# Kernel optimization log

Hardware: AMD Instinct MI355X
Metric: run time of the kernel (lower is better)

Reference implementation:

```python
import jax, jax.numpy as jnp
import numpy as np

T, H, I, E, K = 1024, 1024, 1024, 16, 4
ALPHA, LIMIT, EPS = 1.702, 7.0, 1e-5


def setup_inputs() -> dict:
    key = jax.random.key(0)
    ks = jax.random.split(key, 8)
    return {
        "x": jax.random.normal(ks[0], (T, H), jnp.float32),
        "norm_w": jnp.ones((H,), jnp.float32) + 0.01 * jax.random.normal(ks[1], (H,), jnp.float32),
        "router_w": 0.02 * jax.random.normal(ks[2], (E, H), jnp.float32),
        "router_b": jnp.zeros((E,), jnp.float32),
        "w13": 0.02 * jax.random.normal(ks[3], (E, H, 2 * I), jnp.float32),
        "b13": 0.01 * jax.random.normal(ks[4], (E, 2 * I), jnp.float32),
        "w2": 0.02 * jax.random.normal(ks[5], (E, I, H), jnp.float32),
        "b2": 0.01 * jax.random.normal(ks[6], (E, H), jnp.float32),
        "manual_weights": jnp.zeros((1, E), jnp.float32),  # zeros => override branch inactive, as in __init__
        "layer_idx": 0,
    }


def _override(g, lw):
    # torch: log_softmax, then force pos-masked experts to max+0.01, neg-masked to min-0.01
    gl = jax.nn.log_softmax(g, axis=-1)
    mx = jnp.max(gl, axis=-1, keepdims=True)
    mn = jnp.min(gl, axis=-1, keepdims=True)
    gl = jnp.where((lw > 0)[None, :], mx + 0.01, gl)
    gl = jnp.where((lw < 0)[None, :], mn - 0.01, gl)
    return gl


def reference(x, norm_w, router_w, router_b, w13, b13, w2, b2, manual_weights, layer_idx):
    # RMSNorm (eps=1e-5)
    t = x * jax.lax.rsqrt(jnp.mean(x * x, axis=-1, keepdims=True) + EPS) * norm_w
    # router logits [T, E]
    g = t @ router_w.T + router_b
    # conditional manual logit override
    lw = manual_weights[layer_idx]
    g = jax.lax.cond(jnp.max(jnp.abs(lw)) > 0,
                     lambda gg: _override(gg, lw),
                     lambda gg: gg, g)
    # top-k routing, renormalize=True (softmax -> topk -> renorm)
    probs = jax.nn.softmax(g, axis=-1)
    topw, topi = jax.lax.top_k(probs, K)
    topw = topw / jnp.sum(topw, axis=-1, keepdims=True)
    # dense combine matrix [T, E] (sparse dispatch in the fused kernel)
    combine = jnp.zeros(g.shape, x.dtype).at[jnp.arange(g.shape[0])[:, None], topi].add(topw)
    # expert compute: gate_up GEMM + swigluoai + down GEMM (dense over experts for the reference)
    h = jnp.einsum('th,ehf->tef', t, w13) + b13          # [T, E, 2I]
    gate = jnp.minimum(h[..., :I], LIMIT)                # clamp(max=limit)
    up = jnp.clip(h[..., I:], -LIMIT, LIMIT)             # clamp(-limit, limit)
    act = (up + 1.0) * gate * jax.nn.sigmoid(ALPHA * gate)
    y = jnp.einsum('tei,eih->teh', act, w2) + b2         # [T, E, H]
    moe = jnp.einsum('te,teh->th', combine, y)           # weighted scatter-combine
    return x + moe
```

## Files before the change

kernel.cpp:

```cpp
#include <hip/hip_runtime.h>

#define T_    1024
#define H_    1024
#define IDIM  1024
#define E_    16
#define TOPK  4
#define ALPHA 1.702f
#define LIMIT 7.0f

typedef __bf16 bf16;
typedef __bf16 bf16x4 __attribute__((ext_vector_type(4)));
typedef __bf16 bf16x8 __attribute__((ext_vector_type(8)));
typedef float  f32x4  __attribute__((ext_vector_type(4)));

__global__ __launch_bounds__(256) void k_rms_router(
    const float* __restrict__ x, const float* __restrict__ nw,
    const float* __restrict__ rw, const float* __restrict__ rb,
    const float* __restrict__ mw, const int* __restrict__ lidx,
    bf16* __restrict__ tB, float* __restrict__ out,
    int* __restrict__ cnt, int* __restrict__ tok_list,
    float* __restrict__ wgt_list)
{
    const int t = blockIdx.x, tid = threadIdx.x;
    const int lane = tid & 63, wave = tid >> 6;
    __shared__ float tbuf[H_];
    __shared__ float red[4];
    __shared__ float logits[E_];

    float4 xv = ((const float4*)(x + (size_t)t * H_))[tid];
    float4 wv = ((const float4*)nw)[tid];
    float ssq = xv.x*xv.x + xv.y*xv.y + xv.z*xv.z + xv.w*xv.w;
    #pragma unroll
    for (int off = 32; off; off >>= 1) ssq += __shfl_xor(ssq, off);
    if (lane == 0) red[wave] = ssq;
    __syncthreads();
    const float rms = rsqrtf((red[0] + red[1] + red[2] + red[3]) * (1.0f / H_) + 1e-5f);

    float4 tv;
    tv.x = xv.x * rms * wv.x;
    tv.y = xv.y * rms * wv.y;
    tv.z = xv.z * rms * wv.z;
    tv.w = xv.w * rms * wv.w;

    ((float4*)(out + (size_t)t * H_))[tid] = xv;
    ((float4*)tbuf)[tid] = tv;
    bf16x4 tb = { (bf16)tv.x, (bf16)tv.y, (bf16)tv.z, (bf16)tv.w };
    *(bf16x4*)(tB + (size_t)t * H_ + tid * 4) = tb;
    __syncthreads();

    #pragma unroll
    for (int ei = 0; ei < 4; ++ei) {
        const int e = wave * 4 + ei;
        const float* wr = rw + (size_t)e * H_;
        float s = 0.f;
        #pragma unroll
        for (int j = 0; j < 16; ++j) {
            const int c = lane + j * 64;
            s += tbuf[c] * wr[c];
        }
        #pragma unroll
        for (int off = 32; off; off >>= 1) s += __shfl_xor(s, off);
        if (lane == 0) logits[e] = s + rb[e];
    }
    __syncthreads();

    if (tid == 0) {
        float g[E_];
        #pragma unroll
        for (int e = 0; e < E_; ++e) g[e] = logits[e];

        const int li = lidx[0];
        float ma = 0.f, lw[E_];
        #pragma unroll
        for (int e = 0; e < E_; ++e) { lw[e] = mw[li * E_ + e]; ma = fmaxf(ma, fabsf(lw[e])); }
        if (ma > 0.f) {
            float mx = -1e30f;
            for (int e = 0; e < E_; ++e) mx = fmaxf(mx, g[e]);
            float se = 0.f;
            for (int e = 0; e < E_; ++e) se += expf(g[e] - mx);
            const float lse = logf(se) + mx;
            float gl[E_], gmx = -1e30f, gmn = 1e30f;
            for (int e = 0; e < E_; ++e) { gl[e] = g[e] - lse; gmx = fmaxf(gmx, gl[e]); gmn = fminf(gmn, gl[e]); }
            for (int e = 0; e < E_; ++e) {
                if (lw[e] > 0.f)      gl[e] = gmx + 0.01f;
                else if (lw[e] < 0.f) gl[e] = gmn - 0.01f;
                g[e] = gl[e];
            }
        }

        float mx = -1e30f;
        #pragma unroll
        for (int e = 0; e < E_; ++e) mx = fmaxf(mx, g[e]);
        float p[E_];
        #pragma unroll
        for (int e = 0; e < E_; ++e) p[e] = expf(g[e] - mx);

        bool used[E_] = {};
        int   idx[TOPK];
        float twv[TOPK];
        float ssum = 0.f;
        for (int k = 0; k < TOPK; ++k) {
            int best = -1; float bv = -1e30f;
            for (int e = 0; e < E_; ++e)
                if (!used[e] && p[e] > bv) { bv = p[e]; best = e; }
            used[best] = true; idx[k] = best; twv[k] = bv; ssum += bv;
        }
        const float inv = 1.f / ssum;
        for (int k = 0; k < TOPK; ++k) {
            const int e = idx[k];
            const int slot = atomicAdd(&cnt[e], 1);
            tok_list[e * T_ + slot] = t;
            wgt_list[e * T_ + slot] = twv[k] * inv;
        }
    }
}

__global__ void k_scan(const int* __restrict__ cnt, int* __restrict__ base,
                       int* __restrict__ tiln, int* __restrict__ tile_e,
                       int* __restrict__ tile_m0)
{
    if (threadIdx.x == 0) {
        int s = 0, nt = 0;
        for (int e = 0; e < E_; ++e) {
            base[e] = s; s += cnt[e];
            for (int m0 = 0; m0 < cnt[e]; m0 += 64) {
                if (nt < 96) { tile_e[nt] = e; tile_m0[nt] = m0; ++nt; }
            }
        }
        base[E_] = s;
        tiln[0] = nt;
    }
}

__global__ __launch_bounds__(256) void k_repack(
    const float* __restrict__ W, bf16* __restrict__ out, int Ndim)
{
    __shared__ float tile[32][260];
    const int e = blockIdx.z, kb = blockIdx.y, n0 = blockIdx.x * 256;
    const int t = threadIdx.x;
    const int nbs = Ndim >> 4;

    const float* src = W + ((size_t)e * 1024 + (size_t)kb * 32) * Ndim + n0;
    #pragma unroll
    for (int i = 0; i < 8; ++i) {
        const int idx = i * 256 + t;
        const int k = idx >> 6, c4 = (idx & 63) * 4;
        float4 v = *(const float4*)(src + (size_t)k * Ndim + c4);
        *(float4*)&tile[k][c4] = v;
    }
    __syncthreads();

    const int f = t >> 4;
    const int lg = (t & 15) * 4;
    bf16* dst = out + (((size_t)(e * nbs + n0 / 16 + f)) * 32 + kb) * 512;
    #pragma unroll
    for (int li = 0; li < 4; ++li) {
        const int l = lg + li, q = l >> 4, r = l & 15;
        bf16x8 p;
        #pragma unroll
        for (int j = 0; j < 8; ++j) p[j] = (bf16)tile[q * 8 + j][f * 16 + r];
        *(bf16x8*)(dst + l * 8) = p;
    }
}

__global__ __launch_bounds__(256) void k_gateup3(
    const bf16* __restrict__ tB, const bf16* __restrict__ w13p,
    const float* __restrict__ b13, const int* __restrict__ cnt,
    const int* __restrict__ base, const int* __restrict__ tiln,
    const int* __restrict__ tile_e, const int* __restrict__ tile_m0,
    const int* __restrict__ tok_list, bf16* __restrict__ act)
{
    const int ti = blockIdx.y;
    if (ti >= tiln[0]) return;
    const int e  = tile_e[ti];
    const int m0 = tile_m0[ti];
    const int ne = cnt[e];

    const int tid = threadIdx.x, lane = tid & 63, wave = tid >> 6;
    const int q = lane >> 4, r = lane & 15;

    __shared__ __align__(16) bf16 As[8 * 64 * 8];

    const int m   = tid >> 2, kq = tid & 3;
    const int mf_s = m >> 4, r_s = m & 15;
    const int kc_s = kq >> 1, q_s = (kq & 1) * 2;
    bf16* wr0 = As + ((size_t)((mf_s * 2 + kc_s) * 64 + q_s * 16 + r_s)) * 8;
    bf16* wr1 = wr0 + 16 * 8;
    int srow = m0 + m; srow = srow < ne ? srow : ne - 1;
    const bf16* pA = tB + (size_t)tok_list[e * T_ + srow] * H_ + kq * 16;

    const int nb_g = blockIdx.x * 4 + wave;
    const bf16* pBg = w13p + ((size_t)(e * 128 + nb_g     ) * 32) * 512 + lane * 8;
    const bf16* pBu = w13p + ((size_t)(e * 128 + nb_g + 64) * 32) * 512 + lane * 8;

    f32x4 accg[4] = {};
    f32x4 accu[4] = {};
    uint4 ar0a, ar0b, ar1a, ar1b;
    bf16x8 bg0[2], bu0[2], bg1[2], bu1[2];

#define LOADA(A0, A1) do { \
    A0 = *(const uint4*)pA; A1 = *(const uint4*)(pA + 8); pA += 64; } while (0)
#define STAGEA(A0, A1) do { \
    *(uint4*)wr0 = A0; *(uint4*)wr1 = A1; } while (0)
#define LOADB(BG, BU) do { \
    BG[0] = *(const bf16x8*)pBg; BG[1] = *(const bf16x8*)(pBg + 512); pBg += 1024; \
    BU[0] = *(const bf16x8*)pBu; BU[1] = *(const bf16x8*)(pBu + 512); pBu += 1024; } while (0)
#define COMPUTE(BG, BU) do { \
    _Pragma("unroll") \
    for (int kc = 0; kc < 2; ++kc) { \
        bf16x8 afr[4]; \
        _Pragma("unroll") \
        for (int mf = 0; mf < 4; ++mf) \
            afr[mf] = *(const bf16x8*)(As + ((size_t)((mf * 2 + kc) * 64 + lane)) * 8); \
        _Pragma("unroll") \
        for (int mf = 0; mf < 4; ++mf) { \
            accg[mf] = __builtin_amdgcn_mfma_f32_16x16x32_bf16(afr[mf], BG[kc], accg[mf], 0, 0, 0); \
            accu[mf] = __builtin_amdgcn_mfma_f32_16x16x32_bf16(afr[mf], BU[kc], accu[mf], 0, 0, 0); \
        } \
    } } while (0)

    LOADA(ar0a, ar0b);
    LOADB(bg0, bu0);
    #pragma unroll 2
    for (int kb = 0; kb < 16; kb += 2) {
        __syncthreads();
        STAGEA(ar0a, ar0b);
        LOADA(ar1a, ar1b);
        LOADB(bg1, bu1);
        __syncthreads();
        COMPUTE(bg0, bu0);

        __syncthreads();
        STAGEA(ar1a, ar1b);
        LOADA(ar0a, ar0b);
        LOADB(bg0, bu0);
        __syncthreads();
        COMPUTE(bg1, bu1);
    }
#undef LOADA
#undef STAGEA
#undef LOADB
#undef COMPUTE

    const int sb = base[e];
    const int cg = nb_g * 16 + r;
    const float bgv = b13[e * 2 * IDIM + cg];
    const float buv = b13[e * 2 * IDIM + IDIM + cg];
    #pragma unroll
    for (int mf = 0; mf < 4; ++mf) {
        #pragma unroll
        for (int rg = 0; rg < 4; ++rg) {
            const int row = mf * 16 + q * 4 + rg;
            if (m0 + row < ne) {
                const float hg = accg[mf][rg] + bgv;
                const float hu = accu[mf][rg] + buv;
                const float gt = fminf(hg, LIMIT);
                const float up = fminf(fmaxf(hu, -LIMIT), LIMIT);
                const float av = (up + 1.0f) * gt / (1.0f + expf(-ALPHA * gt));
                act[(size_t)(sb + m0 + row) * IDIM + cg] = (bf16)av;
            }
        }
    }
}

__global__ __launch_bounds__(256) void k_down3(
    const bf16* __restrict__ act, const bf16* __restrict__ w2p,
    const float* __restrict__ b2, const int* __restrict__ cnt,
    const int* __restrict__ base, const int* __restrict__ tiln,
    const int* __restrict__ tile_e, const int* __restrict__ tile_m0,
    const int* __restrict__ tok_list, const float* __restrict__ wgt_list,
    float* __restrict__ out)
{
    const int ti = blockIdx.y;
    if (ti >= tiln[0]) return;
    const int e  = tile_e[ti];
    const int m0 = tile_m0[ti];
    const int ne = cnt[e];
    const int sb = base[e];

    const int tid = threadIdx.x, lane = tid & 63, wave = tid >> 6;
    const int q = lane >> 4, r = lane & 15;

    __shared__ __align__(16) bf16 As[8 * 64 * 8];

    const int m   = tid >> 2, kq = tid & 3;
    const int mf_s = m >> 4, r_s = m & 15;
    const int kc_s = kq >> 1, q_s = (kq & 1) * 2;
    bf16* wr0 = As + ((size_t)((mf_s * 2 + kc_s) * 64 + q_s * 16 + r_s)) * 8;
    bf16* wr1 = wr0 + 16 * 8;
    int srow = m0 + m; srow = srow < ne ? srow : ne - 1;
    const bf16* pA = act + (size_t)(sb + srow) * IDIM + kq * 16;

    const int nb0 = blockIdx.x * 8 + wave * 2;
    const bf16* pB0 = w2p + ((size_t)(e * 64 + nb0    ) * 32) * 512 + lane * 8;
    const bf16* pB1 = w2p + ((size_t)(e * 64 + nb0 + 1) * 32) * 512 + lane * 8;

    f32x4 acc[4][2] = {};
    uint4 ar0a, ar0b, ar1a, ar1b;
    bf16x8 bA0[2], bB0[2], bA1[2], bB1[2];

#define LOADA(A0, A1) do { \
    A0 = *(const uint4*)pA; A1 = *(const uint4*)(pA + 8); pA += 64; } while (0)
#define STAGEA(A0, A1) do { \
    *(uint4*)wr0 = A0; *(uint4*)wr1 = A1; } while (0)
#define LOADB(B0, B1) do { \
    B0[0] = *(const bf16x8*)pB0; B0[1] = *(const bf16x8*)(pB0 + 512); pB0 += 1024; \
    B1[0] = *(const bf16x8*)pB1; B1[1] = *(const bf16x8*)(pB1 + 512); pB1 += 1024; } while (0)
#define COMPUTE(B0, B1) do { \
    _Pragma("unroll") \
    for (int kc = 0; kc < 2; ++kc) { \
        bf16x8 afr[4]; \
        _Pragma("unroll") \
        for (int mf = 0; mf < 4; ++mf) \
            afr[mf] = *(const bf16x8*)(As + ((size_t)((mf * 2 + kc) * 64 + lane)) * 8); \
        _Pragma("unroll") \
        for (int mf = 0; mf < 4; ++mf) { \
            acc[mf][0] = __builtin_amdgcn_mfma_f32_16x16x32_bf16(afr[mf], B0[kc], acc[mf][0], 0, 0, 0); \
            acc[mf][1] = __builtin_amdgcn_mfma_f32_16x16x32_bf16(afr[mf], B1[kc], acc[mf][1], 0, 0, 0); \
        } \
    } } while (0)

    LOADA(ar0a, ar0b);
    LOADB(bA0, bB0);
    #pragma unroll 2
    for (int kb = 0; kb < 16; kb += 2) {
        __syncthreads();
        STAGEA(ar0a, ar0b);
        LOADA(ar1a, ar1b);
        LOADB(bA1, bB1);
        __syncthreads();
        COMPUTE(bA0, bB0);

        __syncthreads();
        STAGEA(ar1a, ar1b);
        LOADA(ar0a, ar0b);
        LOADB(bA0, bB0);
        __syncthreads();
        COMPUTE(bA1, bB1);
    }
#undef LOADA
#undef STAGEA
#undef LOADB
#undef COMPUTE

    #pragma unroll
    for (int nf = 0; nf < 2; ++nf) {
        const int ch = (nb0 + nf) * 16 + r;
        const float bb = b2[e * H_ + ch];
        #pragma unroll
        for (int mf = 0; mf < 4; ++mf) {
            #pragma unroll
            for (int rg = 0; rg < 4; ++rg) {
                const int row = mf * 16 + q * 4 + rg;
                const int s = m0 + row;
                if (s < ne) {
                    const int   tok = tok_list[e * T_ + s];
                    const float w   = wgt_list[e * T_ + s];
                    atomicAdd(&out[(size_t)tok * H_ + ch], w * (acc[mf][nf][rg] + bb));
                }
            }
        }
    }
}

__global__ __launch_bounds__(256) void k_gateup(
    const bf16* __restrict__ tB, const float* __restrict__ w13,
    const float* __restrict__ b13, const int* __restrict__ cnt,
    const int* __restrict__ base, const int* __restrict__ tok_list,
    bf16* __restrict__ act)
{
    const int e  = blockIdx.z;
    const int ne = cnt[e];
    const int m0 = blockIdx.y * 64;
    if (m0 >= ne) return;
    const int n0  = blockIdx.x * 64;
    const int tid = threadIdx.x, lane = tid & 63, wave = tid >> 6;

    __shared__ __align__(16) bf16 As[64][40];
    __shared__ __align__(16) bf16 Bg[64][40];
    __shared__ __align__(16) bf16 Bu[64][40];
    __shared__ int stok[64];

    if (tid < 64) {
        const int s = m0 + tid;
        stok[tid] = (s < ne) ? tok_list[e * T_ + s] : -1;
    }
    __syncthreads();

    const int ar = tid >> 2, ak = (tid & 3) * 8;
    const int atok = stok[ar];
    const int bn = tid & 63, bk = wave * 8;
    const size_t wrow = (size_t)(2 * IDIM);
    const float* wbase = w13 + (size_t)e * H_ * wrow + n0 + bn;

    const int wm = wave >> 1, wn = wave & 1;
    const int q = lane >> 4, r = lane & 15;
    f32x4 accg[2][2] = {};
    f32x4 accu[2][2] = {};

    for (int kb = 0; kb < H_ / 32; ++kb) {
        __syncthreads();
        uint4 av = make_uint4(0u, 0u, 0u, 0u);
        if (atok >= 0)
            av = *(const uint4*)(tB + (size_t)atok * H_ + kb * 32 + ak);
        *(uint4*)&As[ar][ak] = av;
        {
            const float* src = wbase + (size_t)(kb * 32 + bk) * wrow;
            bf16x8 pg, pu;
            #pragma unroll
            for (int j = 0; j < 8; ++j) {
                pg[j] = (bf16)src[(size_t)j * wrow];
                pu[j] = (bf16)src[(size_t)j * wrow + IDIM];
            }
            *(bf16x8*)&Bg[bn][bk] = pg;
            *(bf16x8*)&Bu[bn][bk] = pu;
        }
        __syncthreads();
        bf16x8 a[2], bg[2], bu[2];
        a[0]  = *(const bf16x8*)&As[wm * 32 +      r][q * 8];
        a[1]  = *(const bf16x8*)&As[wm * 32 + 16 + r][q * 8];
        bg[0] = *(const bf16x8*)&Bg[wn * 32 +      r][q * 8];
        bg[1] = *(const bf16x8*)&Bg[wn * 32 + 16 + r][q * 8];
        bu[0] = *(const bf16x8*)&Bu[wn * 32 +      r][q * 8];
        bu[1] = *(const bf16x8*)&Bu[wn * 32 + 16 + r][q * 8];
        #pragma unroll
        for (int im = 0; im < 2; ++im)
            #pragma unroll
            for (int in = 0; in < 2; ++in) {
                accg[im][in] = __builtin_amdgcn_mfma_f32_16x16x32_bf16(a[im], bg[in], accg[im][in], 0, 0, 0);
                accu[im][in] = __builtin_amdgcn_mfma_f32_16x16x32_bf16(a[im], bu[in], accu[im][in], 0, 0, 0);
            }
    }

    const int sb = base[e];
    #pragma unroll
    for (int im = 0; im < 2; ++im)
        #pragma unroll
        for (int in = 0; in < 2; ++in)
            #pragma unroll
            for (int rg = 0; rg < 4; ++rg) {
                const int row = wm * 32 + im * 16 + q * 4 + rg;
                const int col = wn * 32 + in * 16 + r;
                if (m0 + row < ne) {
                    const float hg = accg[im][in][rg] + b13[e * 2 * IDIM + n0 + col];
                    const float hu = accu[im][in][rg] + b13[e * 2 * IDIM + IDIM + n0 + col];
                    const float gt = fminf(hg, LIMIT);
                    const float up = fminf(fmaxf(hu, -LIMIT), LIMIT);
                    const float av = (up + 1.0f) * gt / (1.0f + expf(-ALPHA * gt));
                    act[(size_t)(sb + m0 + row) * IDIM + n0 + col] = (bf16)av;
                }
            }
}

__global__ __launch_bounds__(256) void k_down(
    const bf16* __restrict__ act, const float* __restrict__ w2,
    const float* __restrict__ b2, const int* __restrict__ cnt,
    const int* __restrict__ base, const int* __restrict__ tok_list,
    const float* __restrict__ wgt_list, float* __restrict__ out)
{
    const int e  = blockIdx.z;
    const int ne = cnt[e];
    const int m0 = blockIdx.y * 64;
    if (m0 >= ne) return;
    const int n0  = blockIdx.x * 64;
    const int tid = threadIdx.x, lane = tid & 63, wave = tid >> 6;

    __shared__ __align__(16) bf16 As[64][40];
    __shared__ __align__(16) bf16 Bs[64][40];
    __shared__ int   stok[64];
    __shared__ float swgt[64];

    if (tid < 64) {
        const int s = m0 + tid;
        stok[tid] = (s < ne) ? tok_list[e * T_ + s] : -1;
        swgt[tid] = (s < ne) ? wgt_list[e * T_ + s] : 0.f;
    }
    __syncthreads();

    const int sb = base[e];
    const int ar = tid >> 2, ak = (tid & 3) * 8;
    const bool arow_ok = (m0 + ar) < ne;
    const int bn = tid & 63, bk = wave * 8;
    const float* wbase = w2 + (size_t)e * IDIM * H_ + n0 + bn;

    const int wm = wave >> 1, wn = wave & 1;
    const int q = lane >> 4, r = lane & 15;
    f32x4 acc[2][2] = {};

    for (int kb = 0; kb < IDIM / 32; ++kb) {
        __syncthreads();
        uint4 av = make_uint4(0u, 0u, 0u, 0u);
        if (arow_ok)
            av = *(const uint4*)(act + (size_t)(sb + m0 + ar) * IDIM + kb * 32 + ak);
        *(uint4*)&As[ar][ak] = av;
        {
            const float* src = wbase + (size_t)(kb * 32 + bk) * H_;
            bf16x8 pb;
            #pragma unroll
            for (int j = 0; j < 8; ++j) pb[j] = (bf16)src[(size_t)j * H_];
            *(bf16x8*)&Bs[bn][bk] = pb;
        }
        __syncthreads();
        bf16x8 a[2], b[2];
        a[0] = *(const bf16x8*)&As[wm * 32 +      r][q * 8];
        a[1] = *(const bf16x8*)&As[wm * 32 + 16 + r][q * 8];
        b[0] = *(const bf16x8*)&Bs[wn * 32 +      r][q * 8];
        b[1] = *(const bf16x8*)&Bs[wn * 32 + 16 + r][q * 8];
        #pragma unroll
        for (int im = 0; im < 2; ++im)
            #pragma unroll
            for (int in = 0; in < 2; ++in)
                acc[im][in] = __builtin_amdgcn_mfma_f32_16x16x32_bf16(a[im], b[in], acc[im][in], 0, 0, 0);
    }

    #pragma unroll
    for (int im = 0; im < 2; ++im)
        #pragma unroll
        for (int in = 0; in < 2; ++in)
            #pragma unroll
            for (int rg = 0; rg < 4; ++rg) {
                const int row = wm * 32 + im * 16 + q * 4 + rg;
                const int col = wn * 32 + in * 16 + r;
                if (m0 + row < ne) {
                    const int   tok = stok[row];
                    const float w   = swgt[row];
                    atomicAdd(&out[(size_t)tok * H_ + n0 + col], w * (acc[im][in][rg] + b2[e * H_ + n0 + col]));
                }
            }
}

extern "C" void kernel_launch(void* const* d_in, const int* in_sizes, int n_in,
                              void* d_out, int out_size, void* d_ws, size_t ws_size,
                              hipStream_t stream)
{
    const float* x        = (const float*)d_in[0];
    const float* norm_w   = (const float*)d_in[1];
    const float* router_w = (const float*)d_in[2];
    const float* router_b = (const float*)d_in[3];
    const float* w13      = (const float*)d_in[4];
    const float* b13      = (const float*)d_in[5];
    const float* w2       = (const float*)d_in[6];
    const float* b2       = (const float*)d_in[7];
    const float* manual_w = (const float*)d_in[8];
    const int*   layer_i  = (const int*)d_in[9];
    float* out = (float*)d_out;

    char* ws = (char*)d_ws;
    bf16*  tB   = (bf16*)ws;
    bf16*  act  = (bf16*)(ws + (2ull << 20));
    char*  meta = ws + (10ull << 20);
    int*   cnt      = (int*)meta;
    int*   basep    = (int*)(meta + 64);
    int*   tiln     = (int*)(meta + 256);
    int*   tile_e   = (int*)(meta + 512);
    int*   tile_m0  = (int*)(meta + 1024);
    int*   tok_list = (int*)(meta + (16ull << 10));
    float* wgt_list = (float*)(meta + (16ull << 10) + (64ull << 10));
    bf16*  w13p     = (bf16*)(ws + (12ull << 20));
    bf16*  w2p      = (bf16*)(ws + (76ull << 20));

    const bool fast = ws_size >= (108ull << 20);

    hipMemsetAsync(cnt, 0, E_ * sizeof(int), stream);

    k_rms_router<<<T_, 256, 0, stream>>>(x, norm_w, router_w, router_b,
                                         manual_w, layer_i, tB, out,
                                         cnt, tok_list, wgt_list);
    k_scan<<<1, 64, 0, stream>>>(cnt, basep, tiln, tile_e, tile_m0);

    if (fast) {
        dim3 gr13(2 * IDIM / 256, 32, E_);
        k_repack<<<gr13, 256, 0, stream>>>(w13, w13p, 2 * IDIM);
        dim3 gr2(H_ / 256, 32, E_);
        k_repack<<<gr2, 256, 0, stream>>>(w2, w2p, H_);

        dim3 gg(16, 80);
        k_gateup3<<<gg, 256, 0, stream>>>(tB, w13p, b13, cnt, basep, tiln,
                                          tile_e, tile_m0, tok_list, act);
        dim3 gd(8, 80);
        k_down3<<<gd, 256, 0, stream>>>(act, w2p, b2, cnt, basep, tiln,
                                        tile_e, tile_m0, tok_list, wgt_list, out);
    } else {
        dim3 gg(IDIM / 64, T_ / 64, E_);
        k_gateup<<<gg, 256, 0, stream>>>(tB, w13, b13, cnt, basep, tok_list, act);
        dim3 gd(H_ / 64, T_ / 64, E_);
        k_down<<<gd, 256, 0, stream>>>(act, w2, b2, cnt, basep, tok_list, wgt_list, out);
    }
}
```

Baseline: 402.6 us.

## Drop weight repack kernels and load fp32 weights directly in MoE GEMMs

Removes the two per-call repack kernels that converted the fp32 expert weights into an MFMA-friendly bf16 layout. The GEMM kernels now read the fp32 weights in place with strided scalar loads, converting to bf16 in registers. This saves a full read and write of all weights each call, but replaces vectorized loads with many strided scalar ones. The K loop is peeled so it no longer issues the redundant final prefetch, and the single-thread scan becomes a wave shuffle prefix scan.

Result: slower. 452.3 us (+12.3%).

```diff
diff --git a/kernel.cpp b/kernel.cpp
--- a/kernel.cpp
+++ b/kernel.cpp
@@ -119,52 +119,36 @@
                        int* __restrict__ tiln, int* __restrict__ tile_e,
                        int* __restrict__ tile_m0)
 {
-    if (threadIdx.x == 0) {
-        int s = 0, nt = 0;
-        for (int e = 0; e < E_; ++e) {
-            base[e] = s; s += cnt[e];
-            for (int m0 = 0; m0 < cnt[e]; m0 += 64) {
-                if (nt < 96) { tile_e[nt] = e; tile_m0[nt] = m0; ++nt; }
-            }
-        }
-        base[E_] = s;
-        tiln[0] = nt;
+    const int lane = threadIdx.x;
+    int c = (lane < E_) ? cnt[lane] : 0;
+
+    int s = c;
+    #pragma unroll
+    for (int off = 1; off < 16; off <<= 1) {
+        int tv = __shfl_up(s, off);
+        if ((lane & 15) >= off) s += tv;
+    }
+    if (lane < E_) base[lane] = s - c;
+    if (lane == E_ - 1) base[E_] = s;
+
+    int nt = (lane < E_) ? ((c + 63) >> 6) : 0;
+    int ts = nt;
+    #pragma unroll
+    for (int off = 1; off < 16; off <<= 1) {
+        int tv = __shfl_up(ts, off);
+        if ((lane & 15) >= off) ts += tv;
+    }
+    if (lane == E_ - 1) tiln[0] = ts;
+    if (lane < E_) {
+        const int t0 = ts - nt;
+        for (int i = 0; i < nt; ++i) {
+            if (t0 + i < 96) { tile_e[t0 + i] = lane; tile_m0[t0 + i] = i * 64; }
+        }
     }
 }
 
-__global__ __launch_bounds__(256) void k_repack(
-    const float* __restrict__ W, bf16* __restrict__ out, int Ndim)
-{
-    __shared__ float tile[32][260];
-    const int e = blockIdx.z, kb = blockIdx.y, n0 = blockIdx.x * 256;
-    const int t = threadIdx.x;
-    const int nbs = Ndim >> 4;
-
-    const float* src = W + ((size_t)e * 1024 + (size_t)kb * 32) * Ndim + n0;
-    #pragma unroll
-    for (int i = 0; i < 8; ++i) {
-        const int idx = i * 256 + t;
-        const int k = idx >> 6, c4 = (idx & 63) * 4;
-        float4 v = *(const float4*)(src + (size_t)k * Ndim + c4);
-        *(float4*)&tile[k][c4] = v;
-    }
-    __syncthreads();
-
-    const int f = t >> 4;
-    const int lg = (t & 15) * 4;
-    bf16* dst = out + (((size_t)(e * nbs + n0 / 16 + f)) * 32 + kb) * 512;
-    #pragma unroll
-    for (int li = 0; li < 4; ++li) {
-        const int l = lg + li, q = l >> 4, r = l & 15;
-        bf16x8 p;
-        #pragma unroll
-        for (int j = 0; j < 8; ++j) p[j] = (bf16)tile[q * 8 + j][f * 16 + r];
-        *(bf16x8*)(dst + l * 8) = p;
-    }
-}
-
-__global__ __launch_bounds__(256) void k_gateup3(
-    const bf16* __restrict__ tB, const bf16* __restrict__ w13p,
+__global__ __launch_bounds__(256) void k_gateup4(
+    const bf16* __restrict__ tB, const float* __restrict__ w13,
     const float* __restrict__ b13, const int* __restrict__ cnt,
     const int* __restrict__ base, const int* __restrict__ tiln,
     const int* __restrict__ tile_e, const int* __restrict__ tile_m0,
@@ -190,8 +174,10 @@
     const bf16* pA = tB + (size_t)tok_list[e * T_ + srow] * H_ + kq * 16;
 
     const int nb_g = blockIdx.x * 4 + wave;
-    const bf16* pBg = w13p + ((size_t)(e * 128 + nb_g     ) * 32) * 512 + lane * 8;
-    const bf16* pBu = w13p + ((size_t)(e * 128 + nb_g + 64) * 32) * 512 + lane * 8;
+    const size_t wrow = 2 * IDIM;
+    const float* pBg = w13 + (size_t)e * H_ * wrow + (size_t)(q * 8) * wrow
+                           + (size_t)nb_g * 16 + r;
+    const float* pBu = pBg + IDIM;
 
     f32x4 accg[4] = {};
     f32x4 accu[4] = {};
@@ -203,8 +189,14 @@
 #define STAGEA(A0, A1) do { \
     *(uint4*)wr0 = A0; *(uint4*)wr1 = A1; } while (0)
 #define LOADB(BG, BU) do { \
-    BG[0] = *(const bf16x8*)pBg; BG[1] = *(const bf16x8*)(pBg + 512); pBg += 1024; \
-    BU[0] = *(const bf16x8*)pBu; BU[1] = *(const bf16x8*)(pBu + 512); pBu += 1024; } while (0)
+    _Pragma("unroll") \
+    for (int j = 0; j < 8; ++j) { \
+        BG[0][j] = (bf16)pBg[(size_t)j * wrow]; \
+        BG[1][j] = (bf16)pBg[(size_t)(j + 32) * wrow]; \
+        BU[0][j] = (bf16)pBu[(size_t)j * wrow]; \
+        BU[1][j] = (bf16)pBu[(size_t)(j + 32) * wrow]; \
+    } \
+    pBg += 64 * wrow; pBu += 64 * wrow; } while (0)
 #define COMPUTE(BG, BU) do { \
     _Pragma("unroll") \
     for (int kc = 0; kc < 2; ++kc) { \
@@ -221,8 +213,8 @@
 
     LOADA(ar0a, ar0b);
     LOADB(bg0, bu0);
-    #pragma unroll 2
-    for (int kb = 0; kb < 16; kb += 2) {
+    #pragma unroll 1
+    for (int kb = 0; kb < 14; kb += 2) {
         __syncthreads();
         STAGEA(ar0a, ar0b);
         LOADA(ar1a, ar1b);
@@ -237,6 +229,17 @@
         __syncthreads();
         COMPUTE(bg1, bu1);
     }
+    __syncthreads();
+    STAGEA(ar0a, ar0b);
+    LOADA(ar1a, ar1b);
+    LOADB(bg1, bu1);
+    __syncthreads();
+    COMPUTE(bg0, bu0);
+
+    __syncthreads();
+    STAGEA(ar1a, ar1b);
+    __syncthreads();
+    COMPUTE(bg1, bu1);
 #undef LOADA
 #undef STAGEA
 #undef LOADB
@@ -263,8 +266,8 @@
     }
 }
 
-__global__ __launch_bounds__(256) void k_down3(
-    const bf16* __restrict__ act, const bf16* __restrict__ w2p,
+__global__ __launch_bounds__(256) void k_down4(
+    const bf16* __restrict__ act, const float* __restrict__ w2,
     const float* __restrict__ b2, const int* __restrict__ cnt,
     const int* __restrict__ base, const int* __restrict__ tiln,
     const int* __restrict__ tile_e, const int* __restrict__ tile_m0,
@@ -292,8 +295,9 @@
     const bf16* pA = act + (size_t)(sb + srow) * IDIM + kq * 16;
 
     const int nb0 = blockIdx.x * 8 + wave * 2;
-    const bf16* pB0 = w2p + ((size_t)(e * 64 + nb0    ) * 32) * 512 + lane * 8;
-    const bf16* pB1 = w2p + ((size_t)(e * 64 + nb0 + 1) * 32) * 512 + lane * 8;
+    const float* pB0 = w2 + (size_t)e * IDIM * H_ + (size_t)(q * 8) * H_
+                          + (size_t)nb0 * 16 + r;
+    const float* pB1 = pB0 + 16;
 
     f32x4 acc[4][2] = {};
     uint4 ar0a, ar0b, ar1a, ar1b;
@@ -304,8 +308,14 @@
 #define STAGEA(A0, A1) do { \
     *(uint4*)wr0 = A0; *(uint4*)wr1 = A1; } while (0)
 #define LOADB(B0, B1) do { \
-    B0[0] = *(const bf16x8*)pB0; B0[1] = *(const bf16x8*)(pB0 + 512); pB0 += 1024; \
-    B1[0] = *(const bf16x8*)pB1; B1[1] = *(const bf16x8*)(pB1 + 512); pB1 += 1024; } while (0)
+    _Pragma("unroll") \
+    for (int j = 0; j < 8; ++j) { \
+        B0[0][j] = (bf16)pB0[(size_t)j * H_]; \
+        B0[1][j] = (bf16)pB0[(size_t)(j + 32) * H_]; \
+        B1[0][j] = (bf16)pB1[(size_t)j * H_]; \
+        B1[1][j] = (bf16)pB1[(size_t)(j + 32) * H_]; \
+    } \
+    pB0 += 64 * H_; pB1 += 64 * H_; } while (0)
 #define COMPUTE(B0, B1) do { \
     _Pragma("unroll") \
     for (int kc = 0; kc < 2; ++kc) { \
@@ -322,8 +332,8 @@
 
     LOADA(ar0a, ar0b);
     LOADB(bA0, bB0);
-    #pragma unroll 2
-    for (int kb = 0; kb < 16; kb += 2) {
+    #pragma unroll 1
+    for (int kb = 0; kb < 14; kb += 2) {
         __syncthreads();
         STAGEA(ar0a, ar0b);
         LOADA(ar1a, ar1b);
@@ -338,6 +348,17 @@
         __syncthreads();
         COMPUTE(bA1, bB1);
     }
+    __syncthreads();
+    STAGEA(ar0a, ar0b);
+    LOADA(ar1a, ar1b);
+    LOADB(bA1, bB1);
+    __syncthreads();
+    COMPUTE(bA0, bB0);
+
+    __syncthreads();
+    STAGEA(ar1a, ar1b);
+    __syncthreads();
+    COMPUTE(bA1, bB1);
 #undef LOADA
 #undef STAGEA
 #undef LOADB
@@ -556,10 +577,8 @@
     int*   tile_m0  = (int*)(meta + 1024);
     int*   tok_list = (int*)(meta + (16ull << 10));
     float* wgt_list = (float*)(meta + (16ull << 10) + (64ull << 10));
-    bf16*  w13p     = (bf16*)(ws + (12ull << 20));
-    bf16*  w2p      = (bf16*)(ws + (76ull << 20));
-
-    const bool fast = ws_size >= (108ull << 20);
+
+    const bool fast = ws_size >= (11ull << 20);
 
     hipMemsetAsync(cnt, 0, E_ * sizeof(int), stream);
 
@@ -569,16 +588,11 @@
     k_scan<<<1, 64, 0, stream>>>(cnt, basep, tiln, tile_e, tile_m0);
 
     if (fast) {
-        dim3 gr13(2 * IDIM / 256, 32, E_);
-        k_repack<<<gr13, 256, 0, stream>>>(w13, w13p, 2 * IDIM);
-        dim3 gr2(H_ / 256, 32, E_);
-        k_repack<<<gr2, 256, 0, stream>>>(w2, w2p, H_);
-
         dim3 gg(16, 80);
-        k_gateup3<<<gg, 256, 0, stream>>>(tB, w13p, b13, cnt, basep, tiln,
+        k_gateup4<<<gg, 256, 0, stream>>>(tB, w13, b13, cnt, basep, tiln,
                                           tile_e, tile_m0, tok_list, act);
         dim3 gd(8, 80);
-        k_down3<<<gd, 256, 0, stream>>>(act, w2p, b2, cnt, basep, tiln,
+        k_down4<<<gd, 256, 0, stream>>>(act, w2, b2, cnt, basep, tiln,
                                         tile_e, tile_m0, tok_list, wgt_list, out);
     } else {
         dim3 gg(IDIM / 64, T_ / 64, E_);
```

## Load A fragments directly from global into registers, drop LDS staging and barriers

Applied to the files above, without the earlier changes.

The gate-up and down GEMM kernels no longer stage activation rows through shared memory. Each wave now loads its MFMA A fragments straight from global memory into registers, double-buffered alongside the B loads, which removes four __syncthreads per iteration. The cost is that each wave re-reads the same A rows that other waves in the block also read, increasing global and L2 traffic and register pressure. The single-thread scan kernel is also rewritten as a 16-lane shuffle prefix sum.

Result: slower. 479.2 us (+19.0%).

```diff
diff --git a/kernel.cpp b/kernel.cpp
--- a/kernel.cpp
+++ b/kernel.cpp
@@ -119,16 +119,31 @@
                        int* __restrict__ tiln, int* __restrict__ tile_e,
                        int* __restrict__ tile_m0)
 {
-    if (threadIdx.x == 0) {
-        int s = 0, nt = 0;
-        for (int e = 0; e < E_; ++e) {
-            base[e] = s; s += cnt[e];
-            for (int m0 = 0; m0 < cnt[e]; m0 += 64) {
-                if (nt < 96) { tile_e[nt] = e; tile_m0[nt] = m0; ++nt; }
-            }
-        }
-        base[E_] = s;
-        tiln[0] = nt;
+    const int lane = threadIdx.x;
+    int c = (lane < E_) ? cnt[lane] : 0;
+
+    int s = c;
+    #pragma unroll
+    for (int off = 1; off < 16; off <<= 1) {
+        int tv = __shfl_up(s, off);
+        if ((lane & 15) >= off) s += tv;
+    }
+    if (lane < E_) base[lane] = s - c;
+    if (lane == E_ - 1) base[E_] = s;
+
+    int nt = (lane < E_) ? ((c + 63) >> 6) : 0;
+    int ts = nt;
+    #pragma unroll
+    for (int off = 1; off < 16; off <<= 1) {
+        int tv = __shfl_up(ts, off);
+        if ((lane & 15) >= off) ts += tv;
+    }
+    if (lane == E_ - 1) tiln[0] = ts;
+    if (lane < E_) {
+        const int t0 = ts - nt;
+        for (int i = 0; i < nt; ++i) {
+            if (t0 + i < 96) { tile_e[t0 + i] = lane; tile_m0[t0 + i] = i * 64; }
+        }
     }
 }
 
@@ -163,7 +178,7 @@
     }
 }
 
-__global__ __launch_bounds__(256) void k_gateup3(
+__global__ __launch_bounds__(256) void k_gateup5(
     const bf16* __restrict__ tB, const bf16* __restrict__ w13p,
     const float* __restrict__ b13, const int* __restrict__ cnt,
     const int* __restrict__ base, const int* __restrict__ tiln,
@@ -179,15 +194,13 @@
     const int tid = threadIdx.x, lane = tid & 63, wave = tid >> 6;
     const int q = lane >> 4, r = lane & 15;
 
-    __shared__ __align__(16) bf16 As[8 * 64 * 8];
-
-    const int m   = tid >> 2, kq = tid & 3;
-    const int mf_s = m >> 4, r_s = m & 15;
-    const int kc_s = kq >> 1, q_s = (kq & 1) * 2;
-    bf16* wr0 = As + ((size_t)((mf_s * 2 + kc_s) * 64 + q_s * 16 + r_s)) * 8;
-    bf16* wr1 = wr0 + 16 * 8;
-    int srow = m0 + m; srow = srow < ne ? srow : ne - 1;
-    const bf16* pA = tB + (size_t)tok_list[e * T_ + srow] * H_ + kq * 16;
+    const bf16* pAr[4];
+    #pragma unroll
+    for (int mf = 0; mf < 4; ++mf) {
+        int row = m0 + mf * 16 + r;
+        row = row < ne ? row : ne - 1;
+        pAr[mf] = tB + (size_t)tok_list[e * T_ + row] * H_ + q * 8;
+    }
 
     const int nb_g = blockIdx.x * 4 + wave;
     const bf16* pBg = w13p + ((size_t)(e * 128 + nb_g     ) * 32) * 512 + lane * 8;
@@ -195,51 +208,41 @@
 
     f32x4 accg[4] = {};
     f32x4 accu[4] = {};
-    uint4 ar0a, ar0b, ar1a, ar1b;
-    bf16x8 bg0[2], bu0[2], bg1[2], bu1[2];
-
-#define LOADA(A0, A1) do { \
-    A0 = *(const uint4*)pA; A1 = *(const uint4*)(pA + 8); pA += 64; } while (0)
-#define STAGEA(A0, A1) do { \
-    *(uint4*)wr0 = A0; *(uint4*)wr1 = A1; } while (0)
-#define LOADB(BG, BU) do { \
+    bf16x8 a0[4][2], a1[4][2], bg0[2], bu0[2], bg1[2], bu1[2];
+
+#define LOADS(AF, BG, BU, K0) do { \
+    _Pragma("unroll") \
+    for (int mf = 0; mf < 4; ++mf) { \
+        AF[mf][0] = *(const bf16x8*)(pAr[mf] + (K0)); \
+        AF[mf][1] = *(const bf16x8*)(pAr[mf] + (K0) + 32); \
+    } \
     BG[0] = *(const bf16x8*)pBg; BG[1] = *(const bf16x8*)(pBg + 512); pBg += 1024; \
-    BU[0] = *(const bf16x8*)pBu; BU[1] = *(const bf16x8*)(pBu + 512); pBu += 1024; } while (0)
-#define COMPUTE(BG, BU) do { \
+    BU[0] = *(const bf16x8*)pBu; BU[1] = *(const bf16x8*)(pBu + 512); pBu += 1024; \
+} while (0)
+
+#define COMPUTE(AF, BG, BU) do { \
     _Pragma("unroll") \
-    for (int kc = 0; kc < 2; ++kc) { \
-        bf16x8 afr[4]; \
-        _Pragma("unroll") \
-        for (int mf = 0; mf < 4; ++mf) \
-            afr[mf] = *(const bf16x8*)(As + ((size_t)((mf * 2 + kc) * 64 + lane)) * 8); \
+    for (int kc = 0; kc < 2; ++kc) \
         _Pragma("unroll") \
         for (int mf = 0; mf < 4; ++mf) { \
-            accg[mf] = __builtin_amdgcn_mfma_f32_16x16x32_bf16(afr[mf], BG[kc], accg[mf], 0, 0, 0); \
-            accu[mf] = __builtin_amdgcn_mfma_f32_16x16x32_bf16(afr[mf], BU[kc], accu[mf], 0, 0, 0); \
+            accg[mf] = __builtin_amdgcn_mfma_f32_16x16x32_bf16(AF[mf][kc], BG[kc], accg[mf], 0, 0, 0); \
+            accu[mf] = __builtin_amdgcn_mfma_f32_16x16x32_bf16(AF[mf][kc], BU[kc], accu[mf], 0, 0, 0); \
         } \
-    } } while (0)
-
-    LOADA(ar0a, ar0b);
-    LOADB(bg0, bu0);
-    #pragma unroll 2
-    for (int kb = 0; kb < 16; kb += 2) {
-        __syncthreads();
-        STAGEA(ar0a, ar0b);
-        LOADA(ar1a, ar1b);
-        LOADB(bg1, bu1);
-        __syncthreads();
-        COMPUTE(bg0, bu0);
-
-        __syncthreads();
-        STAGEA(ar1a, ar1b);
-        LOADA(ar0a, ar0b);
-        LOADB(bg0, bu0);
-        __syncthreads();
-        COMPUTE(bg1, bu1);
-    }
-#undef LOADA
-#undef STAGEA
-#undef LOADB
+} while (0)
+
+    LOADS(a0, bg0, bu0, 0);
+    #pragma unroll 1
+    for (int t = 0; t < 7; ++t) {
+        LOADS(a1, bg1, bu1, 64);
+        COMPUTE(a0, bg0, bu0);
+        LOADS(a0, bg0, bu0, 128);
+        COMPUTE(a1, bg1, bu1);
+        pAr[0] += 128; pAr[1] += 128; pAr[2] += 128; pAr[3] += 128;
+    }
+    LOADS(a1, bg1, bu1, 64);
+    COMPUTE(a0, bg0, bu0);
+    COMPUTE(a1, bg1, bu1);
+#undef LOADS
 #undef COMPUTE
 
     const int sb = base[e];
@@ -263,7 +266,7 @@
     }
 }
 
-__global__ __launch_bounds__(256) void k_down3(
+__global__ __launch_bounds__(256) void k_down5(
     const bf16* __restrict__ act, const bf16* __restrict__ w2p,
     const float* __restrict__ b2, const int* __restrict__ cnt,
     const int* __restrict__ base, const int* __restrict__ tiln,
@@ -281,66 +284,54 @@
     const int tid = threadIdx.x, lane = tid & 63, wave = tid >> 6;
     const int q = lane >> 4, r = lane & 15;
 
-    __shared__ __align__(16) bf16 As[8 * 64 * 8];
-
-    const int m   = tid >> 2, kq = tid & 3;
-    const int mf_s = m >> 4, r_s = m & 15;
-    const int kc_s = kq >> 1, q_s = (kq & 1) * 2;
-    bf16* wr0 = As + ((size_t)((mf_s * 2 + kc_s) * 64 + q_s * 16 + r_s)) * 8;
-    bf16* wr1 = wr0 + 16 * 8;
-    int srow = m0 + m; srow = srow < ne ? srow : ne - 1;
-    const bf16* pA = act + (size_t)(sb + srow) * IDIM + kq * 16;
+    const bf16* pAr[4];
+    #pragma unroll
+    for (int mf = 0; mf < 4; ++mf) {
+        int row = m0 + mf * 16 + r;
+        row = row < ne ? row : ne - 1;
+        pAr[mf] = act + (size_t)(sb + row) * IDIM + q * 8;
+    }
 
     const int nb0 = blockIdx.x * 8 + wave * 2;
     const bf16* pB0 = w2p + ((size_t)(e * 64 + nb0    ) * 32) * 512 + lane * 8;
     const bf16* pB1 = w2p + ((size_t)(e * 64 + nb0 + 1) * 32) * 512 + lane * 8;
 
     f32x4 acc[4][2] = {};
-    uint4 ar0a, ar0b, ar1a, ar1b;
-    bf16x8 bA0[2], bB0[2], bA1[2], bB1[2];
-
-#define LOADA(A0, A1) do { \
-    A0 = *(const uint4*)pA; A1 = *(const uint4*)(pA + 8); pA += 64; } while (0)
-#define STAGEA(A0, A1) do { \
-    *(uint4*)wr0 = A0; *(uint4*)wr1 = A1; } while (0)
-#define LOADB(B0, B1) do { \
+    bf16x8 a0[4][2], a1[4][2], c0[2], d0[2], c1[2], d1[2];
+
+#define LOADS(AF, B0, B1, K0) do { \
+    _Pragma("unroll") \
+    for (int mf = 0; mf < 4; ++mf) { \
+        AF[mf][0] = *(const bf16x8*)(pAr[mf] + (K0)); \
+        AF[mf][1] = *(const bf16x8*)(pAr[mf] + (K0) + 32); \
+    } \
     B0[0] = *(const bf16x8*)pB0; B0[1] = *(const bf16x8*)(pB0 + 512); pB0 += 1024; \
-    B1[0] = *(const bf16x8*)pB1; B1[1] = *(const bf16x8*)(pB1 + 512); pB1 += 1024; } while (0)
-#define COMPUTE(B0, B1) do { \
+    B1[0] = *(const bf16x8*)pB1; B1[1] = *(const bf16x8*)(pB1 + 512); pB1 += 1024; \
+} while (0)
+
+#define COMPUTE(AF, B0, B1) do { \
     _Pragma("unroll") \
-    for (int kc = 0; kc < 2; ++kc) { \
-        bf16x8 afr[4]; \
-        _Pragma("unroll") \
-        for (int mf = 0; mf < 4; ++mf) \
-            afr[mf] = *(const bf16x8*)(As + ((size_t)((mf * 2 + kc) * 64 + lane)) * 8); \
+    for (int kc = 0; kc < 2; ++kc) \
         _Pragma("unroll") \
         for (int mf = 0; mf < 4; ++mf) { \
-            acc[mf][0] = __builtin_amdgcn_mfma_f32_16x16x32_bf16(afr[mf], B0[kc], acc[mf][0], 0, 0, 0); \
-            acc[mf][1] = __builtin_amdgcn_mfma_f32_16x16x32_bf16(afr[mf], B1[kc], acc[mf][1], 0, 0, 0); \
+            acc[mf][0] = __builtin_amdgcn_mfma_f32_16x16x32_bf16(AF[mf][kc], B0[kc], acc[mf][0], 0, 0, 0); \
+            acc[mf][1] = __builtin_amdgcn_mfma_f32_16x16x32_bf16(AF[mf][kc], B1[kc], acc[mf][1], 0, 0, 0); \
         } \
-    } } while (0)
-
-    LOADA(ar0a, ar0b);
-    LOADB(bA0, bB0);
-    #pragma unroll 2
-    for (int kb = 0; kb < 16; kb += 2) {
-        __syncthreads();
-        STAGEA(ar0a, ar0b);
-        LOADA(ar1a, ar1b);
-        LOADB(bA1, bB1);
-        __syncthreads();
-        COMPUTE(bA0, bB0);
-
-        __syncthreads();
-        STAGEA(ar1a, ar1b);
-        LOADA(ar0a, ar0b);
-        LOADB(bA0, bB0);
-        __syncthreads();
-        COMPUTE(bA1, bB1);
-    }
-#undef LOADA
-#undef STAGEA
-#undef LOADB
+} while (0)
+
+    LOADS(a0, c0, d0, 0);
+    #pragma unroll 1
+    for (int t = 0; t < 7; ++t) {
+        LOADS(a1, c1, d1, 64);
+        COMPUTE(a0, c0, d0);
+        LOADS(a0, c0, d0, 128);
+        COMPUTE(a1, c1, d1);
+        pAr[0] += 128; pAr[1] += 128; pAr[2] += 128; pAr[3] += 128;
+    }
+    LOADS(a1, c1, d1, 64);
+    COMPUTE(a0, c0, d0);
+    COMPUTE(a1, c1, d1);
+#undef LOADS
 #undef COMPUTE
 
     #pragma unroll
@@ -575,10 +566,10 @@
         k_repack<<<gr2, 256, 0, stream>>>(w2, w2p, H_);
 
         dim3 gg(16, 80);
-        k_gateup3<<<gg, 256, 0, stream>>>(tB, w13p, b13, cnt, basep, tiln,
+        k_gateup5<<<gg, 256, 0, stream>>>(tB, w13p, b13, cnt, basep, tiln,
                                           tile_e, tile_m0, tok_list, act);
         dim3 gd(8, 80);
-        k_down3<<<gd, 256, 0, stream>>>(act, w2p, b2, cnt, basep, tiln,
+        k_down5<<<gd, 256, 0, stream>>>(act, w2p, b2, cnt, basep, tiln,
                                         tile_e, tile_m0, tok_list, wgt_list, out);
     } else {
         dim3 gg(IDIM / 64, T_ / 64, E_);
```

## Deepen B-operand prefetch, use lgkm-only barriers, parallelize tile scan

Applied to the files above, without the earlier changes.

Both expert GEMM kernels now prefetch weight fragments two k-steps ahead, issuing the next B load right after each compute. Their __syncthreads calls become a custom barrier that waits only on LDS counters, so outstanding global loads are not drained at every sync. The single-thread scan kernel becomes a 16-lane wavefront prefix scan over expert counts and tile counts. The aim is to hide global-memory latency behind MFMA work and to shorten the serial scan, at the cost of more live registers and reliance on the compiler inserting the vmcnt waits needed before the prefetched registers are used.

New measurement: 401.7 us. Within noise of the previous version (-0.2%).

```diff
diff --git a/kernel.cpp b/kernel.cpp
--- a/kernel.cpp
+++ b/kernel.cpp
@@ -12,6 +12,10 @@
 typedef __bf16 bf16x4 __attribute__((ext_vector_type(4)));
 typedef __bf16 bf16x8 __attribute__((ext_vector_type(8)));
 typedef float  f32x4  __attribute__((ext_vector_type(4)));
+
+#define BARRIER() do { \
+    asm volatile("s_waitcnt lgkmcnt(0)" ::: "memory"); \
+    __builtin_amdgcn_s_barrier(); } while (0)
 
 __global__ __launch_bounds__(256) void k_rms_router(
     const float* __restrict__ x, const float* __restrict__ nw,
@@ -119,16 +123,31 @@
                        int* __restrict__ tiln, int* __restrict__ tile_e,
                        int* __restrict__ tile_m0)
 {
-    if (threadIdx.x == 0) {
-        int s = 0, nt = 0;
-        for (int e = 0; e < E_; ++e) {
-            base[e] = s; s += cnt[e];
-            for (int m0 = 0; m0 < cnt[e]; m0 += 64) {
-                if (nt < 96) { tile_e[nt] = e; tile_m0[nt] = m0; ++nt; }
-            }
-        }
-        base[E_] = s;
-        tiln[0] = nt;
+    const int lane = threadIdx.x;
+    int c = (lane < E_) ? cnt[lane] : 0;
+
+    int s = c;
+    #pragma unroll
+    for (int off = 1; off < 16; off <<= 1) {
+        int tv = __shfl_up(s, off);
+        if ((lane & 15) >= off) s += tv;
+    }
+    if (lane < E_) base[lane] = s - c;
+    if (lane == E_ - 1) base[E_] = s;
+
+    int nt = (lane < E_) ? ((c + 63) >> 6) : 0;
+    int ts = nt;
+    #pragma unroll
+    for (int off = 1; off < 16; off <<= 1) {
+        int tv = __shfl_up(ts, off);
+        if ((lane & 15) >= off) ts += tv;
+    }
+    if (lane == E_ - 1) tiln[0] = ts;
+    if (lane < E_) {
+        const int t0 = ts - nt;
+        for (int i = 0; i < nt; ++i) {
+            if (t0 + i < 96) { tile_e[t0 + i] = lane; tile_m0[t0 + i] = i * 64; }
+        }
     }
 }
 
@@ -190,8 +209,8 @@
     const bf16* pA = tB + (size_t)tok_list[e * T_ + srow] * H_ + kq * 16;
 
     const int nb_g = blockIdx.x * 4 + wave;
-    const bf16* pBg = w13p + ((size_t)(e * 128 + nb_g     ) * 32) * 512 + lane * 8;
-    const bf16* pBu = w13p + ((size_t)(e * 128 + nb_g + 64) * 32) * 512 + lane * 8;
+    const bf16* pBg0 = w13p + ((size_t)(e * 128 + nb_g     ) * 32) * 512 + lane * 8;
+    const bf16* pBu0 = w13p + ((size_t)(e * 128 + nb_g + 64) * 32) * 512 + lane * 8;
 
     f32x4 accg[4] = {};
     f32x4 accu[4] = {};
@@ -202,9 +221,12 @@
     A0 = *(const uint4*)pA; A1 = *(const uint4*)(pA + 8); pA += 64; } while (0)
 #define STAGEA(A0, A1) do { \
     *(uint4*)wr0 = A0; *(uint4*)wr1 = A1; } while (0)
-#define LOADB(BG, BU) do { \
-    BG[0] = *(const bf16x8*)pBg; BG[1] = *(const bf16x8*)(pBg + 512); pBg += 1024; \
-    BU[0] = *(const bf16x8*)pBu; BU[1] = *(const bf16x8*)(pBu + 512); pBu += 1024; } while (0)
+#define LOADB(BG, BU, s) do { \
+    const int ss_ = (s) < 16 ? (s) : 15; \
+    BG[0] = *(const bf16x8*)(pBg0 + (size_t)ss_ * 1024); \
+    BG[1] = *(const bf16x8*)(pBg0 + (size_t)ss_ * 1024 + 512); \
+    BU[0] = *(const bf16x8*)(pBu0 + (size_t)ss_ * 1024); \
+    BU[1] = *(const bf16x8*)(pBu0 + (size_t)ss_ * 1024 + 512); } while (0)
 #define COMPUTE(BG, BU) do { \
     _Pragma("unroll") \
     for (int kc = 0; kc < 2; ++kc) { \
@@ -220,22 +242,23 @@
     } } while (0)
 
     LOADA(ar0a, ar0b);
-    LOADB(bg0, bu0);
-    #pragma unroll 2
+    LOADB(bg0, bu0, 0);
+    LOADB(bg1, bu1, 1);
+    #pragma unroll 1
     for (int kb = 0; kb < 16; kb += 2) {
-        __syncthreads();
+        BARRIER();
         STAGEA(ar0a, ar0b);
         LOADA(ar1a, ar1b);
-        LOADB(bg1, bu1);
-        __syncthreads();
+        BARRIER();
         COMPUTE(bg0, bu0);
-
-        __syncthreads();
+        LOADB(bg0, bu0, kb + 2);
+
+        BARRIER();
         STAGEA(ar1a, ar1b);
         LOADA(ar0a, ar0b);
-        LOADB(bg0, bu0);
-        __syncthreads();
+        BARRIER();
         COMPUTE(bg1, bu1);
+        LOADB(bg1, bu1, kb + 3);
     }
 #undef LOADA
 #undef STAGEA
@@ -292,8 +315,8 @@
     const bf16* pA = act + (size_t)(sb + srow) * IDIM + kq * 16;
 
     const int nb0 = blockIdx.x * 8 + wave * 2;
-    const bf16* pB0 = w2p + ((size_t)(e * 64 + nb0    ) * 32) * 512 + lane * 8;
-    const bf16* pB1 = w2p + ((size_t)(e * 64 + nb0 + 1) * 32) * 512 + lane * 8;
+    const bf16* pB0b = w2p + ((size_t)(e * 64 + nb0    ) * 32) * 512 + lane * 8;
+    const bf16* pB1b = w2p + ((size_t)(e * 64 + nb0 + 1) * 32) * 512 + lane * 8;
 
     f32x4 acc[4][2] = {};
     uint4 ar0a, ar0b, ar1a, ar1b;
@@ -303,9 +326,12 @@
     A0 = *(const uint4*)pA; A1 = *(const uint4*)(pA + 8); pA += 64; } while (0)
 #define STAGEA(A0, A1) do { \
     *(uint4*)wr0 = A0; *(uint4*)wr1 = A1; } while (0)
-#define LOADB(B0, B1) do { \
-    B0[0] = *(const bf16x8*)pB0; B0[1] = *(const bf16x8*)(pB0 + 512); pB0 += 1024; \
-    B1[0] = *(const bf16x8*)pB1; B1[1] = *(const bf16x8*)(pB1 + 512); pB1 += 1024; } while (0)
+#define LOADB(B0, B1, s) do { \
+    const int ss_ = (s) < 16 ? (s) : 15; \
+    B0[0] = *(const bf16x8*)(pB0b + (size_t)ss_ * 1024); \
+    B0[1] = *(const bf16x8*)(pB0b + (size_t)ss_ * 1024 + 512); \
+    B1[0] = *(const bf16x8*)(pB1b + (size_t)ss_ * 1024); \
+    B1[1] = *(const bf16x8*)(pB1b + (size_t)ss_ * 1024 + 512); } while (0)
 #define COMPUTE(B0, B1) do { \
     _Pragma("unroll") \
     for (int kc = 0; kc < 2; ++kc) { \
@@ -321,22 +347,23 @@
     } } while (0)
 
     LOADA(ar0a, ar0b);
-    LOADB(bA0, bB0);
-    #pragma unroll 2
+    LOADB(bA0, bB0, 0);
+    LOADB(bA1, bB1, 1);
+    #pragma unroll 1
     for (int kb = 0; kb < 16; kb += 2) {
-        __syncthreads();
+        BARRIER();
         STAGEA(ar0a, ar0b);
         LOADA(ar1a, ar1b);
-        LOADB(bA1, bB1);
-        __syncthreads();
+        BARRIER();
         COMPUTE(bA0, bB0);
-
-        __syncthreads();
+        LOADB(bA0, bB0, kb + 2);
+
+        BARRIER();
         STAGEA(ar1a, ar1b);
         LOADA(ar0a, ar0b);
-        LOADB(bA0, bB0);
-        __syncthreads();
+        BARRIER();
         COMPUTE(bA1, bB1);
+        LOADB(bA1, bB1, kb + 3);
     }
 #undef LOADA
 #undef STAGEA
```
